# Optimization experiments

Measured on AMD Instinct MI355X. Metric: run time of the kernel, lower is better.

The kernel has to match this reference:

```python
import jax, jax.numpy as jnp
import numpy as np

G = 4        # number of grids (batch)
L = 16384    # voxels per grid (equal-length grids)
P = 512      # patch_size
H = 8        # num_heads


def setup_inputs() -> dict:
    key = jax.random.key(0)
    k1, k2, k3, k4, k5, k6 = jax.random.split(key, 6)
    N, C = G * L, 512
    feats = jax.random.normal(k1, (N, C), dtype=jnp.float32)
    curve_codes = jax.random.randint(k2, (N,), 0, 1 << 30, dtype=jnp.int64)
    Wqkv = jax.random.normal(k3, (3 * C, C), dtype=jnp.float32) * 0.02
    bqkv = jax.random.normal(k4, (3 * C,), dtype=jnp.float32) * 0.02
    Wproj = jax.random.normal(k5, (C, C), dtype=jnp.float32) * 0.02
    bproj = jax.random.normal(k6, (C,), dtype=jnp.float32) * 0.02
    return {"feats": feats, "curve_codes": curve_codes, "Wqkv": Wqkv,
            "bqkv": bqkv, "Wproj": Wproj, "bproj": bproj}


def reference(feats, curve_codes, Wqkv, bqkv, Wproj, bproj):
    N, C = feats.shape
    D = C // H
    scale = D ** -0.5
    # per-grid space-filling-curve sort -> global permutation indices
    codes = curve_codes.reshape(G, L)
    perm = (jnp.argsort(codes, axis=1) + jnp.arange(G)[:, None] * L).reshape(N)
    x = feats[perm]                                   # curve-sorted voxels
    qkv = x @ Wqkv.T + bqkv                           # [N, 3C]
    # contiguous patches of size P (grid lengths divisible by P)
    qkv = qkv.reshape(N // P, P, 3, H, D)
    q, k, v = qkv[:, :, 0], qkv[:, :, 1], qkv[:, :, 2]  # [nP, P, H, D]
    scores = jnp.einsum('nphd,nqhd->nhpq', q, k) * scale
    attn = jax.nn.softmax(scores, axis=-1)
    out = jnp.einsum('nhpq,nqhd->nphd', attn, v).reshape(N, C)
    # inverse permutation: out_final[perm[j]] = out[j]
    out = jnp.zeros_like(out).at[perm].set(out)
    return out @ Wproj.T + bproj
```

## Files before the change

### kernel.cpp

```cpp
#include <hip/hip_runtime.h>
#include <hip/hip_bf16.h>


typedef unsigned long long u64;
typedef unsigned short ushort_t;
typedef __attribute__((ext_vector_type(8))) short short8v;
typedef __attribute__((ext_vector_type(4))) float f32x4;

#define MFMA_BF16 __builtin_amdgcn_mfma_f32_16x16x32_bf16

__device__ __forceinline__ unsigned short f2bf(float f) {
  union { float f; unsigned u; } v; v.f = f;
  return (unsigned short)((v.u + 0x7FFFu + ((v.u >> 16) & 1u)) >> 16);
}

__device__ __forceinline__ unsigned pk2(float a, float b) {
  __hip_bfloat162 h = __float22bfloat162_rn(float2{a, b});
  unsigned u; __builtin_memcpy(&u, &h, 4); return u;
}

__device__ __forceinline__ void async16(ushort_t* lds, const ushort_t* g) {
  __builtin_amdgcn_global_load_lds(
      (const __attribute__((address_space(1))) unsigned int*)g,
      (__attribute__((address_space(3))) unsigned int*)lds, 16, 0, 0);
}


__global__ __launch_bounds__(512) void sort_chunk(const int* __restrict__ codes,
                                                  u64* __restrict__ keys) {
  __shared__ u64 sk[2048];
  const int base = blockIdx.x * 2048;
  for (int t = threadIdx.x; t < 2048; t += 512) {
    int e = base + t;
    sk[t] = (((u64)(unsigned)codes[e]) << 14) | (u64)(e & 16383);
  }
  __syncthreads();
  for (int k = 2; k <= 2048; k <<= 1) {
    for (int j = k >> 1; j > 0; j >>= 1) {
      for (int t = threadIdx.x; t < 2048; t += 512) {
        int jx = t ^ j;
        if (jx > t) {
          bool up = (((base + t) & 16383 & k) == 0);
          u64 a = sk[t], b = sk[jx];
          if ((a > b) == up) { sk[t] = b; sk[jx] = a; }
        }
      }
      __syncthreads();
    }
  }
  for (int t = threadIdx.x; t < 2048; t += 512) keys[base + t] = sk[t];
}

__global__ __launch_bounds__(256) void sort_gpass(u64* __restrict__ keys, int k, int j) {
  int t = blockIdx.x * 256 + threadIdx.x;
  int jx = t ^ j;
  if (jx > t) {
    bool up = ((t & 16383 & k) == 0);
    u64 a = keys[t], b = keys[jx];
    if ((a > b) == up) { keys[t] = b; keys[jx] = a; }
  }
}

__global__ __launch_bounds__(512) void sort_finish(u64* __restrict__ keys, int k) {
  __shared__ u64 sk[4096];
  const int base = blockIdx.x * 4096;
  for (int t = threadIdx.x; t < 4096; t += 512) sk[t] = keys[base + t];
  __syncthreads();
  int j0 = (k >> 1 < 2048) ? (k >> 1) : 2048;
  for (int j = j0; j > 0; j >>= 1) {
    for (int t = threadIdx.x; t < 4096; t += 512) {
      int jx = t ^ j;
      if (jx > t) {
        bool up = (((base + t) & 16383 & k) == 0);
        u64 a = sk[t], b = sk[jx];
        if ((a > b) == up) { sk[t] = b; sk[jx] = a; }
      }
    }
    __syncthreads();
  }
  for (int t = threadIdx.x; t < 4096; t += 512) keys[base + t] = sk[t];
}

__global__ __launch_bounds__(512) void sort_finish_last(const u64* __restrict__ keys,
                                                        int* __restrict__ perm) {
  __shared__ u64 sk[4096];
  const int base = blockIdx.x * 4096;
  const int g = blockIdx.x >> 2;
  for (int t = threadIdx.x; t < 4096; t += 512) sk[t] = keys[base + t];
  __syncthreads();
  for (int j = 2048; j > 0; j >>= 1) {
    for (int t = threadIdx.x; t < 4096; t += 512) {
      int jx = t ^ j;
      if (jx > t) {
        u64 a = sk[t], b = sk[jx];
        if (a > b) { sk[t] = b; sk[jx] = a; }
      }
    }
    __syncthreads();
  }
  for (int t = threadIdx.x; t < 4096; t += 512)
    perm[base + t] = (g << 14) | (int)(sk[t] & 16383);
}


__global__ __launch_bounds__(256) void gather_bf16(const float* __restrict__ feats,
    const int* __restrict__ perm, ushort_t* __restrict__ A) {
  int t = blockIdx.x * 256 + threadIdx.x;
  int m = t >> 5;
  int off = (t & 31) << 4;
  const float* src = feats + (size_t)perm[m] * 512 + off;
  float4 a = ((const float4*)src)[0];
  float4 b = ((const float4*)src)[1];
  float4 c = ((const float4*)src)[2];
  float4 d = ((const float4*)src)[3];
  short8v lo = { (short)f2bf(a.x), (short)f2bf(a.y), (short)f2bf(a.z), (short)f2bf(a.w),
                 (short)f2bf(b.x), (short)f2bf(b.y), (short)f2bf(b.z), (short)f2bf(b.w) };
  short8v hi = { (short)f2bf(c.x), (short)f2bf(c.y), (short)f2bf(c.z), (short)f2bf(c.w),
                 (short)f2bf(d.x), (short)f2bf(d.y), (short)f2bf(d.z), (short)f2bf(d.w) };
  ushort_t* dst = A + (size_t)m * 512 + off;
  *(short8v*)(dst) = lo;
  *(short8v*)(dst + 8) = hi;
}

__global__ __launch_bounds__(256) void convert_both(const float* __restrict__ wq,
    const float* __restrict__ wp, ushort_t* __restrict__ dq, ushort_t* __restrict__ dp) {
  int t = blockIdx.x * 256 + threadIdx.x;
  const float* s;
  ushort_t* d;
  int i;
  if (t < 98304) { s = wq; d = dq; i = t; }
  else           { s = wp; d = dp; i = t - 98304; }
  const float* sp = s + (size_t)i * 8;
  float4 a = ((const float4*)sp)[0];
  float4 b = ((const float4*)sp)[1];
  short8v v = { (short)f2bf(a.x), (short)f2bf(a.y), (short)f2bf(a.z), (short)f2bf(a.w),
                (short)f2bf(b.x), (short)f2bf(b.y), (short)f2bf(b.z), (short)f2bf(b.w) };
  *(short8v*)(d + (size_t)i * 8) = v;
}


__global__ __launch_bounds__(256) void qkv_gemm(const ushort_t* __restrict__ A,
    const ushort_t* __restrict__ W, const float* __restrict__ bias,
    ushort_t* __restrict__ Q, ushort_t* __restrict__ Ko, ushort_t* __restrict__ Vt)
{
  __shared__ __align__(16) ushort_t la[128 * 64];
  __shared__ __align__(16) ushort_t lb[128 * 64];
  const int bid = blockIdx.x;
  const int swz = (bid & 7) * 768 + (bid >> 3);
  const int bx = swz % 12, by = swz / 12;
  const int rowBase = by * 128, colBase = bx * 128;
  const int tid = threadIdx.x, lane = tid & 63, w = tid >> 6;
  const int wr = w >> 1, wc = w & 1;
  const int li = lane & 15, kb = lane >> 4;
  const int lr = lane >> 3;
  const int lcs = (((lane & 7) ^ lr) << 3);
  f32x4 acc[4][4] = {};
  for (int kt = 0; kt < 8; ++kt) {
#pragma unroll
    for (int i = 0; i < 4; ++i) {
      int c = w * 4 + i;
      async16(la + c * 512, A + (size_t)(rowBase + c * 8 + lr) * 512 + kt * 64 + lcs);
      async16(lb + c * 512, W + (size_t)(colBase + c * 8 + lr) * 512 + kt * 64 + lcs);
    }
    __syncthreads();
    short8v af[2][4], bfr[2][4];
#pragma unroll
    for (int kk = 0; kk < 2; ++kk)
#pragma unroll
      for (int t = 0; t < 4; ++t) {
        int sl = ((kk * 4 + kb) ^ (li & 7)) << 3;
        af[kk][t]  = *(const short8v*)(la + (wr * 64 + t * 16 + li) * 64 + sl);
        bfr[kk][t] = *(const short8v*)(lb + (wc * 64 + t * 16 + li) * 64 + sl);
      }
#pragma unroll
    for (int kk = 0; kk < 2; ++kk)
#pragma unroll
      for (int i = 0; i < 4; ++i)
#pragma unroll
        for (int j = 0; j < 4; ++j)
          acc[i][j] = MFMA_BF16(af[kk][i], bfr[kk][j], acc[i][j], 0, 0, 0);
    __syncthreads();
  }
  const int c0 = colBase + wc * 64;
  ushort_t* tw = (w < 2) ? (la + w * 4096) : (lb + (w - 2) * 4096);
  if (c0 >= 1024) {
    char* twb = (char*)tw;
#pragma unroll
    for (int j = 0; j < 4; ++j) {
      int dloc = j * 16 + li;
      float bv = bias[c0 + dloc];
#pragma unroll
      for (int i = 0; i < 4; ++i) {
        unsigned u0 = pk2(acc[i][j][0] + bv, acc[i][j][1] + bv);
        unsigned u1 = pk2(acc[i][j][2] + bv, acc[i][j][3] + bv);
        int s = i * 2 + (kb >> 1);
        int byte = dloc * 128 + ((s ^ (dloc & 7)) << 4) + ((kb & 1) << 3);
        *(uint2*)(twb + byte) = make_uint2(u0, u1);
      }
    }
    const int h = (c0 - 1024) >> 6;
    const size_t nh = (size_t)((rowBase >> 9) * 8 + h);
    const int pbase = ((rowBase + wr * 64) & 511) + ((lane & 7) << 3);
    ushort_t* vb = Vt + nh * 32768 + pbase;
#pragma unroll
    for (int ps = 0; ps < 8; ++ps) {
      int dloc = ps * 8 + (lane >> 3);
      int byte = dloc * 128 + ((((lane & 7)) ^ (dloc & 7)) << 4);
      short8v vv = *(const short8v*)(twb + byte);
      *(short8v*)(vb + dloc * 512) = vv;
    }
  } else {
    const bool isQ = (c0 >> 9) == 0;
    const float qs = isQ ? 0.180336879f : 1.0f;
    unsigned* twd = (unsigned*)tw;
#pragma unroll
    for (int j = 0; j < 4; ++j) {
      int dl = j * 16 + li;
      float bv = bias[c0 + dl];
#pragma unroll
      for (int i = 0; i < 4; ++i)
#pragma unroll
        for (int r = 0; r < 4; ++r) {
          int p = i * 16 + kb * 4 + r;
          unsigned short hv = f2bf((acc[i][j][r] + bv) * qs);
          int dw = (dl >> 1) ^ (kb << 3);
          *((ushort_t*)(twd + p * 32 + dw) + (dl & 1)) = hv;
        }
    }
    const int hq = (c0 >> 6) & 7;
    const size_t nh = (size_t)((rowBase >> 9) * 8 + hq);
    const int p0w = (rowBase + wr * 64) & 511;
    ushort_t* qb = (isQ ? Q : Ko) + (nh * 512 + p0w) * 64 + ((lane & 7) << 3);
    const int prow = lane >> 3;
#pragma unroll
    for (int ps = 0; ps < 8; ++ps) {
      int p = ps * 8 + prow;
      int dw0 = ((lane & 7) << 2) ^ ((((p >> 2) & 3)) << 3);
      short8v vv = *(const short8v*)(twd + p * 32 + dw0);
      *(short8v*)(qb + (size_t)p * 64) = vv;
    }
  }
}


#define TILE_EXP(S, LACC, PB) do {                                             \
  _Pragma("unroll")                                                            \
  for (int t = 0; t < 4; ++t)                                                  \
    _Pragma("unroll")                                                          \
    for (int r = 0; r < 4; ++r) S[t][r] = exp2f(S[t][r]);                      \
  float q0 = (S[0][0] + S[0][1]) + (S[0][2] + S[0][3]);                        \
  float q1 = (S[1][0] + S[1][1]) + (S[1][2] + S[1][3]);                        \
  float q2 = (S[2][0] + S[2][1]) + (S[2][2] + S[2][3]);                        \
  float q3 = (S[3][0] + S[3][1]) + (S[3][2] + S[3][3]);                        \
  LACC += (q0 + q1) + (q2 + q3);                                               \
  _Pragma("unroll")                                                            \
  for (int t = 0; t < 4; ++t) {                                                \
    unsigned plo = pk2(S[t][0], S[t][1]);                                      \
    unsigned phi = pk2(S[t][2], S[t][3]);                                      \
    *(uint2*)((char*)(PB) + (((2 * t + (kb >> 1)) << 8) | (li << 4) |          \
                             ((kb & 1) << 3))) = make_uint2(plo, phi);         \
  }                                                                            \
} while (0)

__global__ __launch_bounds__(256, 2) void attn_kernel(const ushort_t* __restrict__ Q,
    const ushort_t* __restrict__ K, const ushort_t* __restrict__ Vt,
    const int* __restrict__ perm, ushort_t* __restrict__ O)
{
  __shared__ __align__(16) ushort_t kbuf[2][64][64];
  __shared__ __align__(16) ushort_t vbuf[2][64][64];
  __shared__ __align__(16) ushort_t pbuf[4][1024];
  const int b = blockIdx.x;
  const int qc = (b >> 3) & 3;
  const int nh = ((b >> 5) << 3) | (b & 7);
  const int n = nh >> 3, h = nh & 7;
  const int tid = threadIdx.x, w = tid >> 6, lane = tid & 63;
  const int li = lane & 15, kb = lane >> 4;
  const ushort_t* Qb = Q + (size_t)nh * (512 * 64);
  const ushort_t* Kb = K + (size_t)nh * (512 * 64);
  const ushort_t* Vb = Vt + (size_t)nh * (64 * 512);
  const int p0 = qc * 128 + w * 32;

  const int srow = lane >> 3;
  const int ssw = (((lane & 7) ^ srow) << 3);
  const ushort_t* Ksrc = Kb + (size_t)(w * 8 + srow) * 64 + ssw;
  const ushort_t* Vsrc = Vb + (size_t)(w * 8 + srow) * 512 + ssw;

  short8v qa0 = *(const short8v*)(Qb + (size_t)(p0 + li) * 64 + kb * 8);
  short8v qa1 = *(const short8v*)(Qb + (size_t)(p0 + li) * 64 + 32 + kb * 8);
  short8v qb0 = *(const short8v*)(Qb + (size_t)(p0 + 16 + li) * 64 + kb * 8);
  short8v qb1 = *(const short8v*)(Qb + (size_t)(p0 + 16 + li) * 64 + 32 + kb * 8);

  f32x4 oa[4] = {}, ob[4] = {};
  float la_ = 0.f, lb_ = 0.f;
  ushort_t* pb = &pbuf[w][0];
  const int sl0 = (kb ^ (li & 7)) << 3;
  const int sl1 = ((kb + 4) ^ (li & 7)) << 3;
  const char* prd0 = (const char*)pb + ((kb << 8) | (li << 4));
  const char* prd1 = (const char*)pb + (((kb + 4) << 8) | (li << 4));

  async16(&kbuf[0][w * 8][0], Ksrc);
  async16(&kbuf[0][w * 8 + 32][0], Ksrc + 2048);
  async16(&vbuf[0][w * 8][0], Vsrc);
  async16(&vbuf[0][w * 8 + 32][0], Vsrc + 16384);
  __syncthreads();

#pragma unroll 1
  for (int ch = 0; ch < 8; ++ch) {
    const int bi = ch & 1;
    if (ch < 7) {
      async16(&kbuf[bi ^ 1][w * 8][0], Ksrc + (size_t)(ch + 1) * 4096);
      async16(&kbuf[bi ^ 1][w * 8 + 32][0], Ksrc + (size_t)(ch + 1) * 4096 + 2048);
      async16(&vbuf[bi ^ 1][w * 8][0], Vsrc + (ch + 1) * 64);
      async16(&vbuf[bi ^ 1][w * 8 + 32][0], Vsrc + (ch + 1) * 64 + 16384);
    }
    f32x4 sA[4], sB[4];
#pragma unroll
    for (int t = 0; t < 4; ++t) {
      short8v kf0 = *(const short8v*)(&kbuf[bi][t * 16 + li][sl0]);
      short8v kf1 = *(const short8v*)(&kbuf[bi][t * 16 + li][sl1]);
      f32x4 zA = {0.f, 0.f, 0.f, 0.f}, zB = {0.f, 0.f, 0.f, 0.f};
      zA = MFMA_BF16(kf0, qa0, zA, 0, 0, 0);
      zB = MFMA_BF16(kf0, qb0, zB, 0, 0, 0);
      zA = MFMA_BF16(kf1, qa1, zA, 0, 0, 0);
      zB = MFMA_BF16(kf1, qb1, zB, 0, 0, 0);
      sA[t] = zA; sB[t] = zB;
    }
    short8v pa0, pa1, pb0, pb1;
    TILE_EXP(sA, la_, pb);
    pa0 = *(const short8v*)(prd0);
    pa1 = *(const short8v*)(prd1);
    TILE_EXP(sB, lb_, pb);
    pb0 = *(const short8v*)(prd0);
    pb1 = *(const short8v*)(prd1);
    __builtin_amdgcn_s_setprio(1);
#pragma unroll
    for (int dt = 0; dt < 4; ++dt) {
      short8v vf0 = *(const short8v*)(&vbuf[bi][dt * 16 + li][sl0]);
      short8v vf1 = *(const short8v*)(&vbuf[bi][dt * 16 + li][sl1]);
      oa[dt] = MFMA_BF16(pa0, vf0, oa[dt], 0, 0, 0);
      oa[dt] = MFMA_BF16(pa1, vf1, oa[dt], 0, 0, 0);
      ob[dt] = MFMA_BF16(pb0, vf0, ob[dt], 0, 0, 0);
      ob[dt] = MFMA_BF16(pb1, vf1, ob[dt], 0, 0, 0);
    }
    __builtin_amdgcn_s_setprio(0);
    __syncthreads();
    __builtin_amdgcn_sched_barrier(0);
  }
  la_ += __shfl_xor(la_, 16, 64);
  la_ += __shfl_xor(la_, 32, 64);
  lb_ += __shfl_xor(lb_, 16, 64);
  lb_ += __shfl_xor(lb_, 32, 64);
  {
    float iv = 1.0f / la_;
    float iv4[4];
#pragma unroll
    for (int r = 0; r < 4; ++r) iv4[r] = __shfl(iv, (kb << 2) + r, 16);
    int op[4];
#pragma unroll
    for (int r = 0; r < 4; ++r) op[r] = perm[n * 512 + p0 + kb * 4 + r];
#pragma unroll
    for (int dt = 0; dt < 4; ++dt)
#pragma unroll
      for (int r = 0; r < 4; ++r)
        O[(size_t)op[r] * 512 + h * 64 + dt * 16 + li] = f2bf(oa[dt][r] * iv4[r]);
  }
  {
    float iv = 1.0f / lb_;
    float iv4[4];
#pragma unroll
    for (int r = 0; r < 4; ++r) iv4[r] = __shfl(iv, (kb << 2) + r, 16);
    int op[4];
#pragma unroll
    for (int r = 0; r < 4; ++r) op[r] = perm[n * 512 + p0 + 16 + kb * 4 + r];
#pragma unroll
    for (int dt = 0; dt < 4; ++dt)
#pragma unroll
      for (int r = 0; r < 4; ++r)
        O[(size_t)op[r] * 512 + h * 64 + dt * 16 + li] = f2bf(ob[dt][r] * iv4[r]);
  }
}


__global__ __launch_bounds__(256) void proj_gemm(const ushort_t* __restrict__ A,
    const ushort_t* __restrict__ W, const float* __restrict__ bias,
    float* __restrict__ out)
{
  __shared__ __align__(16) ushort_t la[128 * 64];
  __shared__ __align__(16) ushort_t lb[128 * 64];
  const int bid = blockIdx.x;
  const int swz = (bid & 7) * 256 + (bid >> 3);
  const int bx = swz & 3, by = swz >> 2;
  const int rowBase = by * 128, colBase = bx * 128;
  const int tid = threadIdx.x, lane = tid & 63, w = tid >> 6;
  const int wr = w >> 1, wc = w & 1;
  const int li = lane & 15, kb = lane >> 4;
  const int lr = lane >> 3;
  const int lcs = (((lane & 7) ^ lr) << 3);
  f32x4 acc[4][4] = {};
  for (int kt = 0; kt < 8; ++kt) {
#pragma unroll
    for (int i = 0; i < 4; ++i) {
      int c = w * 4 + i;
      async16(la + c * 512, A + (size_t)(rowBase + c * 8 + lr) * 512 + kt * 64 + lcs);
      async16(lb + c * 512, W + (size_t)(colBase + c * 8 + lr) * 512 + kt * 64 + lcs);
    }
    __syncthreads();
    short8v af[2][4], bfr[2][4];
#pragma unroll
    for (int kk = 0; kk < 2; ++kk)
#pragma unroll
      for (int t = 0; t < 4; ++t) {
        int sl = ((kk * 4 + kb) ^ (li & 7)) << 3;
        af[kk][t]  = *(const short8v*)(la + (wr * 64 + t * 16 + li) * 64 + sl);
        bfr[kk][t] = *(const short8v*)(lb + (wc * 64 + t * 16 + li) * 64 + sl);
      }
#pragma unroll
    for (int kk = 0; kk < 2; ++kk)
#pragma unroll
      for (int i = 0; i < 4; ++i)
#pragma unroll
        for (int j = 0; j < 4; ++j)
          acc[i][j] = MFMA_BF16(af[kk][i], bfr[kk][j], acc[i][j], 0, 0, 0);
    __syncthreads();
  }
#pragma unroll
  for (int i = 0; i < 4; ++i)
#pragma unroll
    for (int j = 0; j < 4; ++j) {
      int col = colBase + wc * 64 + j * 16 + li;
      float bv = bias[col];
#pragma unroll
      for (int r = 0; r < 4; ++r) {
        int m = rowBase + wr * 64 + i * 16 + kb * 4 + r;
        out[(size_t)m * 512 + col] = acc[i][j][r] + bv;
      }
    }
}


extern "C" void kernel_launch(void* const* d_in, const int* in_sizes, int n_in,
                              void* d_out, int out_size, void* d_ws, size_t ws_size,
                              hipStream_t stream) {
  (void)in_sizes; (void)n_in; (void)out_size; (void)ws_size;
  const float* feats      = (const float*)d_in[0];
  const int* codes        = (const int*)d_in[1];
  const float* Wqkv       = (const float*)d_in[2];
  const float* bqkv       = (const float*)d_in[3];
  const float* Wproj      = (const float*)d_in[4];
  const float* bproj      = (const float*)d_in[5];
  float* out = (float*)d_out;

  char* ws = (char*)d_ws;
  int* perm = (int*)(ws);
  u64* keys = (u64*)(ws + 262144);
  ushort_t* Abf     = (ushort_t*)(ws + 1048576);
  ushort_t* att     = Abf;
  ushort_t* Wqkvbf  = (ushort_t*)(ws + 1048576 + 67108864);
  ushort_t* Wprojbf = (ushort_t*)(ws + 1048576 + 67108864 + 1572864);
  ushort_t* Qb      = (ushort_t*)(ws + 1048576 + 67108864 + 2097152);
  ushort_t* Kb      = Qb + 33554432ull;
  ushort_t* Vt      = Kb + 33554432ull;

  sort_chunk<<<32, 512, 0, stream>>>(codes, keys);
  sort_finish<<<16, 512, 0, stream>>>(keys, 4096);
  sort_gpass<<<256, 256, 0, stream>>>(keys, 8192, 4096);
  sort_finish<<<16, 512, 0, stream>>>(keys, 8192);
  sort_gpass<<<256, 256, 0, stream>>>(keys, 16384, 8192);
  sort_gpass<<<256, 256, 0, stream>>>(keys, 16384, 4096);
  sort_finish_last<<<16, 512, 0, stream>>>(keys, perm);

  gather_bf16<<<8192, 256, 0, stream>>>(feats, perm, Abf);
  convert_both<<<512, 256, 0, stream>>>(Wqkv, Wproj, Wqkvbf, Wprojbf);

  qkv_gemm<<<6144, 256, 0, stream>>>(Abf, Wqkvbf, bqkv, Qb, Kb, Vt);
  attn_kernel<<<4096, 256, 0, stream>>>(Qb, Kb, Vt, perm, att);
  proj_gemm<<<2048, 256, 0, stream>>>(att, Wprojbf, bproj, out);
}
```

Measured before the change: 400.3 us.

## Double-buffer LDS tiles in QKV and projection GEMMs to overlap loads with MFMA

New measurement: 433.1 us. 8.2% more time.

```diff
diff --git a/kernel.cpp b/kernel.cpp
--- a/kernel.cpp
+++ b/kernel.cpp
@@ -143,8 +143,8 @@
     const ushort_t* __restrict__ W, const float* __restrict__ bias,
     ushort_t* __restrict__ Q, ushort_t* __restrict__ Ko, ushort_t* __restrict__ Vt)
 {
-  __shared__ __align__(16) ushort_t la[128 * 64];
-  __shared__ __align__(16) ushort_t lb[128 * 64];
+  __shared__ __align__(16) ushort_t la[2][128 * 64];
+  __shared__ __align__(16) ushort_t lb[2][128 * 64];
   const int bid = blockIdx.x;
   const int swz = (bid & 7) * 768 + (bid >> 3);
   const int bx = swz % 12, by = swz / 12;
@@ -155,22 +155,42 @@
   const int lr = lane >> 3;
   const int lcs = (((lane & 7) ^ lr) << 3);
   f32x4 acc[4][4] = {};
+#pragma unroll
+  for (int i = 0; i < 4; ++i) {
+    int c = w * 4 + i;
+    async16(&la[0][c * 512], A + (size_t)(rowBase + c * 8 + lr) * 512 + lcs);
+    async16(&lb[0][c * 512], W + (size_t)(colBase + c * 8 + lr) * 512 + lcs);
+  }
+#pragma unroll 1
   for (int kt = 0; kt < 8; ++kt) {
-#pragma unroll
-    for (int i = 0; i < 4; ++i) {
-      int c = w * 4 + i;
-      async16(la + c * 512, A + (size_t)(rowBase + c * 8 + lr) * 512 + kt * 64 + lcs);
-      async16(lb + c * 512, W + (size_t)(colBase + c * 8 + lr) * 512 + kt * 64 + lcs);
-    }
-    __syncthreads();
+    const int cur = kt & 1;
+    if (kt < 7) {
+#pragma unroll
+      for (int i = 0; i < 4; ++i) {
+        int c = w * 4 + i;
+        async16(&la[cur ^ 1][c * 512],
+                A + (size_t)(rowBase + c * 8 + lr) * 512 + (kt + 1) * 64 + lcs);
+        async16(&lb[cur ^ 1][c * 512],
+                W + (size_t)(colBase + c * 8 + lr) * 512 + (kt + 1) * 64 + lcs);
+      }
+      __builtin_amdgcn_sched_barrier(0);
+      asm volatile("s_waitcnt vmcnt(8)" ::: "memory");
+    } else {
+      __builtin_amdgcn_sched_barrier(0);
+      asm volatile("s_waitcnt vmcnt(0)" ::: "memory");
+    }
+    __builtin_amdgcn_s_barrier();
+    __builtin_amdgcn_sched_barrier(0);
+    const ushort_t* lap = la[cur];
+    const ushort_t* lbp = lb[cur];
     short8v af[2][4], bfr[2][4];
 #pragma unroll
     for (int kk = 0; kk < 2; ++kk)
 #pragma unroll
       for (int t = 0; t < 4; ++t) {
         int sl = ((kk * 4 + kb) ^ (li & 7)) << 3;
-        af[kk][t]  = *(const short8v*)(la + (wr * 64 + t * 16 + li) * 64 + sl);
-        bfr[kk][t] = *(const short8v*)(lb + (wc * 64 + t * 16 + li) * 64 + sl);
+        af[kk][t]  = *(const short8v*)(lap + (wr * 64 + t * 16 + li) * 64 + sl);
+        bfr[kk][t] = *(const short8v*)(lbp + (wc * 64 + t * 16 + li) * 64 + sl);
       }
 #pragma unroll
     for (int kk = 0; kk < 2; ++kk)
@@ -179,10 +199,12 @@
 #pragma unroll
         for (int j = 0; j < 4; ++j)
           acc[i][j] = MFMA_BF16(af[kk][i], bfr[kk][j], acc[i][j], 0, 0, 0);
-    __syncthreads();
+    __builtin_amdgcn_sched_barrier(0);
+    __builtin_amdgcn_s_barrier();
+    __builtin_amdgcn_sched_barrier(0);
   }
   const int c0 = colBase + wc * 64;
-  ushort_t* tw = (w < 2) ? (la + w * 4096) : (lb + (w - 2) * 4096);
+  ushort_t* tw = (w < 2) ? (&la[0][0] + w * 4096) : (&lb[0][0] + (w - 2) * 4096);
   if (c0 >= 1024) {
     char* twb = (char*)tw;
 #pragma unroll
@@ -385,8 +407,8 @@
     const ushort_t* __restrict__ W, const float* __restrict__ bias,
     float* __restrict__ out)
 {
-  __shared__ __align__(16) ushort_t la[128 * 64];
-  __shared__ __align__(16) ushort_t lb[128 * 64];
+  __shared__ __align__(16) ushort_t la[2][128 * 64];
+  __shared__ __align__(16) ushort_t lb[2][128 * 64];
   const int bid = blockIdx.x;
   const int swz = (bid & 7) * 256 + (bid >> 3);
   const int bx = swz & 3, by = swz >> 2;
@@ -397,22 +419,42 @@
   const int lr = lane >> 3;
   const int lcs = (((lane & 7) ^ lr) << 3);
   f32x4 acc[4][4] = {};
+#pragma unroll
+  for (int i = 0; i < 4; ++i) {
+    int c = w * 4 + i;
+    async16(&la[0][c * 512], A + (size_t)(rowBase + c * 8 + lr) * 512 + lcs);
+    async16(&lb[0][c * 512], W + (size_t)(colBase + c * 8 + lr) * 512 + lcs);
+  }
+#pragma unroll 1
   for (int kt = 0; kt < 8; ++kt) {
-#pragma unroll
-    for (int i = 0; i < 4; ++i) {
-      int c = w * 4 + i;
-      async16(la + c * 512, A + (size_t)(rowBase + c * 8 + lr) * 512 + kt * 64 + lcs);
-      async16(lb + c * 512, W + (size_t)(colBase + c * 8 + lr) * 512 + kt * 64 + lcs);
-    }
-    __syncthreads();
+    const int cur = kt & 1;
+    if (kt < 7) {
+#pragma unroll
+      for (int i = 0; i < 4; ++i) {
+        int c = w * 4 + i;
+        async16(&la[cur ^ 1][c * 512],
+                A + (size_t)(rowBase + c * 8 + lr) * 512 + (kt + 1) * 64 + lcs);
+        async16(&lb[cur ^ 1][c * 512],
+                W + (size_t)(colBase + c * 8 + lr) * 512 + (kt + 1) * 64 + lcs);
+      }
+      __builtin_amdgcn_sched_barrier(0);
+      asm volatile("s_waitcnt vmcnt(8)" ::: "memory");
+    } else {
+      __builtin_amdgcn_sched_barrier(0);
+      asm volatile("s_waitcnt vmcnt(0)" ::: "memory");
+    }
+    __builtin_amdgcn_s_barrier();
+    __builtin_amdgcn_sched_barrier(0);
+    const ushort_t* lap = la[cur];
+    const ushort_t* lbp = lb[cur];
     short8v af[2][4], bfr[2][4];
 #pragma unroll
     for (int kk = 0; kk < 2; ++kk)
 #pragma unroll
       for (int t = 0; t < 4; ++t) {
         int sl = ((kk * 4 + kb) ^ (li & 7)) << 3;
-        af[kk][t]  = *(const short8v*)(la + (wr * 64 + t * 16 + li) * 64 + sl);
-        bfr[kk][t] = *(const short8v*)(lb + (wc * 64 + t * 16 + li) * 64 + sl);
+        af[kk][t]  = *(const short8v*)(lap + (wr * 64 + t * 16 + li) * 64 + sl);
+        bfr[kk][t] = *(const short8v*)(lbp + (wc * 64 + t * 16 + li) * 64 + sl);
       }
 #pragma unroll
     for (int kk = 0; kk < 2; ++kk)
@@ -421,7 +463,9 @@
 #pragma unroll
         for (int j = 0; j < 4; ++j)
           acc[i][j] = MFMA_BF16(af[kk][i], bfr[kk][j], acc[i][j], 0, 0, 0);
-    __syncthreads();
+    __builtin_amdgcn_sched_barrier(0);
+    __builtin_amdgcn_s_barrier();
+    __builtin_amdgcn_sched_barrier(0);
   }
 #pragma unroll
   for (int i = 0; i < 4; ++i)
```
